# Optimization experiments

Hardware: AMD Instinct MI355X
Metric: run time of the kernel (lower is better)

The kernel has to match this reference:

```python
import jax, jax.numpy as jnp
import numpy as np

MARGIN = 0.5
POS_WEIGHT = 0.5
NEG_WEIGHT = 0.5
PUNISHMENT_SCALE = 2.0
POS_THRESHOLD = 0.6
NEG_THRESHOLD = 0.3
BIG = 1e9  # finite sentinel instead of inf (grad-safe under where)


def setup_inputs() -> dict:
    key = jax.random.key(0)
    k1, k2, k3 = jax.random.split(key, 3)
    N, D = 8192, 256
    embeddings = jax.random.normal(k1, (N, D), dtype=jnp.float32)
    labels = jax.random.randint(k2, (N,), 0, 2, dtype=jnp.int32)
    pids = jax.random.randint(k3, (N,), 0, 256, dtype=jnp.int32)
    return {"embeddings": embeddings, "labels": labels, "pids": pids}


def reference(embeddings, labels, pids):
    N = embeddings.shape[0]
    # F.normalize(p=2, dim=1): x / max(||x||, eps)
    norm = jnp.maximum(jnp.linalg.norm(embeddings, axis=1, keepdims=True), 1e-12)
    normed = embeddings / norm
    sim = normed @ normed.T  # (N, N) cosine similarity

    same_pid = pids[:, None] == pids[None, :]            # (N, N)
    genuine_j = (labels == 1)[None, :]                   # (1, N)
    not_self = ~jnp.eye(N, dtype=bool)
    pos_mask = same_pid & genuine_j & not_self           # same pid, genuine, not anchor
    neg_mask = (same_pid & ~genuine_j) | ~same_pid       # same-pid forgeries or cross-pid

    valid = (labels == 1) & pos_mask.any(axis=1) & neg_mask.any(axis=1)

    # hardest positive = min similarity among positives
    hp = jnp.min(jnp.where(pos_mask, sim, BIG), axis=1)  # (N,)

    # semi-hard negatives: hp - margin < sim < hp
    semi = neg_mask & (sim < hp[:, None]) & (sim > (hp - MARGIN)[:, None])
    cand = neg_mask & (sim > hp[:, None])                # harder-than-positive negatives
    hn_semi = jnp.max(jnp.where(semi, sim, -BIG), axis=1)
    hn_cand = jnp.max(jnp.where(cand, sim, -BIG), axis=1)
    hn_all = jnp.max(jnp.where(neg_mask, sim, -BIG), axis=1)
    hn = jnp.where(semi.any(axis=1), hn_semi,
                   jnp.where(cand.any(axis=1), hn_cand, hn_all))

    base = jax.nn.relu(hn - hp + MARGIN)
    weight = jnp.where((hp < POS_THRESHOLD) | (hn > NEG_THRESHOLD),
                       PUNISHMENT_SCALE, 1.0)
    loss = base * weight + POS_WEIGHT * (1.0 - hp) + NEG_WEIGHT * jax.nn.relu(hn + 0.2)

    cnt = jnp.sum(valid)
    total = jnp.sum(jnp.where(valid, loss, 0.0))
    return jnp.where(cnt > 0, total / jnp.maximum(cnt, 1), 0.0)
```

## Files before the change

### kernel.cpp

```cpp
#include <hip/hip_runtime.h>
#include <hip/hip_bf16.h>
#include <stdint.h>

typedef __attribute__((ext_vector_type(8))) short short8;
typedef __attribute__((ext_vector_type(4))) float f32x4;

#define BIGF 1e9f
#define NSLOT 64
#define MAXM 96

__device__ inline float blo(unsigned int u) {
    union { unsigned int i; float f; } v; v.i = u << 16; return v.f;
}
__device__ inline float bhi(unsigned int u) {
    union { unsigned int i; float f; } v; v.i = u & 0xffff0000u; return v.f;
}
__device__ inline unsigned int fkey(float s) {
    unsigned int b = __float_as_uint(s);
    return (b & 0x80000000u) ? ~b : (b | 0x80000000u);
}
__device__ inline float funkey(unsigned int k) {
    unsigned int b = (k & 0x80000000u) ? (k & 0x7fffffffu) : ~k;
    return __uint_as_float(b);
}
__device__ inline void async16(const unsigned short* g, unsigned short* l) {
    __builtin_amdgcn_global_load_lds(
        (const __attribute__((address_space(1))) void*)g,
        (__attribute__((address_space(3))) void*)l, 16, 0, 0);
}
__device__ inline unsigned short f2b(float x) {
    __hip_bfloat16 h = __float2bfloat16(x);
    return *reinterpret_cast<unsigned short*>(&h);
}

__global__ __launch_bounds__(256) void k_normalize(
    const float* __restrict__ emb, const int* __restrict__ labels,
    const int* __restrict__ pids, unsigned short* __restrict__ normed,
    int* __restrict__ pg, float* __restrict__ hp_init,
    float* __restrict__ gred, int* __restrict__ done)
{
    if (blockIdx.x == 0 && threadIdx.x < 3) {
        if (threadIdx.x < 2) gred[threadIdx.x] = 0.f;
        else *done = 0;
    }
    int w = threadIdx.x >> 6, lane = threadIdx.x & 63;
    int row = blockIdx.x * 4 + w;
    const float4* src = (const float4*)(emb + ((size_t)row << 8));
    float4 x = src[lane];
    float ss = x.x * x.x + x.y * x.y + x.z * x.z + x.w * x.w;
    #pragma unroll
    for (int off = 32; off >= 1; off >>= 1) ss += __shfl_xor(ss, off, 64);
    float inv = 1.0f / fmaxf(sqrtf(ss), 1e-12f);
    ushort4 o;
    o.x = f2b(x.x * inv); o.y = f2b(x.y * inv);
    o.z = f2b(x.z * inv); o.w = f2b(x.w * inv);
    ((ushort4*)(normed + ((size_t)row << 8)))[lane] = o;
    if (lane == 0) {
        int g = (labels[row] == 1) ? pids[row] : -1;
        pg[row] = (pids[row] & 0xffff) | ((g + 1) << 16);
        hp_init[row] = BIGF;
    }
}

__global__ __launch_bounds__(256) void k_hp_pid(
    const unsigned short* __restrict__ normed, const int* __restrict__ labels,
    const int* __restrict__ pids, float* __restrict__ hp_out, int N, int D)
{
    __shared__ int list[MAXM];
    __shared__ unsigned int hp_loc[MAXM];
    __shared__ unsigned short rows[MAXM * 256];
    __shared__ int cnt;
    int p = blockIdx.x;
    int t = threadIdx.x;
    if (t == 0) cnt = 0;
    __syncthreads();
    for (int j = t; j < N; j += 256)
        if (pids[j] == p && labels[j] == 1) {
            int idx = atomicAdd(&cnt, 1);
            if (idx < MAXM) list[idx] = j;
        }
    __syncthreads();
    int M = min(cnt, MAXM);
    for (int s = t; s < M; s += 256) hp_loc[s] = 0xFFFFFFFFu;
    for (int idx = t; idx < M * 32; idx += 256) {
        int mi = idx >> 5, ch = idx & 31;
        ((uint4*)&rows[mi * 256])[ch] =
            ((const uint4*)(normed + ((size_t)list[mi] << 8)))[ch];
    }
    __syncthreads();
    for (int pr = t; pr < M * M; pr += 256) {
        int i = pr / M, j = pr - i * M;
        if (i == j) continue;
        const uint4* ap = (const uint4*)&rows[i * 256];
        const uint4* bp = (const uint4*)&rows[j * 256];
        float s = 0.f;
        #pragma unroll 4
        for (int k = 0; k < 32; ++k) {
            uint4 a = ap[k], b = bp[k];
            s += blo(a.x) * blo(b.x) + bhi(a.x) * bhi(b.x);
            s += blo(a.y) * blo(b.y) + bhi(a.y) * bhi(b.y);
            s += blo(a.z) * blo(b.z) + bhi(a.z) * bhi(b.z);
            s += blo(a.w) * blo(b.w) + bhi(a.w) * bhi(b.w);
        }
        atomicMin(&hp_loc[i], fkey(s));
    }
    __syncthreads();
    for (int s = t; s < M; s += 256) {
        unsigned int key = hp_loc[s];
        hp_out[list[s]] = (key == 0xFFFFFFFFu) ? BIGF : funkey(key);
    }
}

__global__ __launch_bounds__(512) void k_pass2(
    const unsigned short* __restrict__ normed, const int* __restrict__ pg,
    const float* __restrict__ hp,
    float* __restrict__ p_hnall, float* __restrict__ p_mbel, int N)
{
    const int b = blockIdx.x;
    int rt, ct;
    if (b >= 2016) {
        rt = b - 2016; ct = rt;
    } else {
        int r = (int)floorf((127.0f - sqrtf(16129.0f - 8.0f * (float)b)) * 0.5f);
        r = max(0, min(r, 62));
        while (63 * (r + 1) - ((r + 1) * r) / 2 <= b) ++r;
        while (63 * r - (r * (r - 1)) / 2 > b) --r;
        rt = r;
        ct = r + 1 + (b - (63 * r - (r * (r - 1)) / 2));
    }
    const bool diag = (ct == rt);

    __shared__ unsigned short As[2][128 * 32];
    __shared__ unsigned short Bs[2][128 * 32];
    __shared__ float hp_r[128], hp_c[128];
    __shared__ int pg_r[128], pg_c[128];
    __shared__ unsigned int red1[128], red2[128], red3[128], red4[128];

    const int t = threadIdx.x;
    const int lane = t & 63;
    const int w = t >> 6;
    const int wr = w & 3, wc = w >> 2;
    const int quad = lane >> 4, l16 = lane & 15;
    const int rbase = rt * 128, cbase = ct * 128;

    if (t < 128) {
        hp_r[t] = hp[rbase + t];
        pg_r[t] = pg[rbase + t];
        hp_c[t] = hp[cbase + t];
        pg_c[t] = pg[cbase + t];
        red1[t] = 0u; red2[t] = 0u; red3[t] = 0u; red4[t] = 0u;
    }

    const int r0 = t >> 2, p0 = t & 3;
    const int c0 = p0 ^ ((r0 >> 1) & 3);
    const unsigned short* gA = normed + ((size_t)(rbase + r0) << 8) + c0 * 8;
    const unsigned short* gB = normed + ((size_t)(cbase + r0) << 8) + c0 * 8;

    async16(gA, &As[0][t * 8]);
    if (!diag) async16(gB, &Bs[0][t * 8]);

    f32x4 acc[2][4];
    #pragma unroll
    for (int mt = 0; mt < 2; ++mt)
        #pragma unroll
        for (int nt = 0; nt < 4; ++nt)
            acc[mt][nt] = (f32x4){0.f, 0.f, 0.f, 0.f};

    const int sw = (l16 >> 1) & 3;
    const int aoff = (wr * 32 + l16) * 32 + (quad ^ sw) * 8;
    const int boff = (wc * 64 + l16) * 32 + (quad ^ sw) * 8;
    const unsigned short* Bbase[2] = { diag ? &As[0][0] : &Bs[0][0],
                                       diag ? &As[1][0] : &Bs[1][0] };

    for (int kb = 0; kb < 8; ++kb) {
        __syncthreads();
        int cur = kb & 1;
        if (kb < 7) {
            int nxt = cur ^ 1;
            int ko = (kb + 1) << 5;
            async16(gA + ko, &As[nxt][t * 8]);
            if (!diag) async16(gB + ko, &Bs[nxt][t * 8]);
        }
        short8 af[2], bf[4];
        #pragma unroll
        for (int mt = 0; mt < 2; ++mt)
            af[mt] = *reinterpret_cast<const short8*>(&As[cur][aoff + mt * 512]);
        #pragma unroll
        for (int nt = 0; nt < 4; ++nt)
            bf[nt] = *reinterpret_cast<const short8*>(&Bbase[cur][boff + nt * 512]);
        #pragma unroll
        for (int mt = 0; mt < 2; ++mt)
            #pragma unroll
            for (int nt = 0; nt < 4; ++nt)
                acc[mt][nt] = __builtin_amdgcn_mfma_f32_16x16x32_bf16(
                    af[mt], bf[nt], acc[mt][nt], 0, 0, 0);
    }

    {
        const unsigned int gp0 = ((unsigned int)pg_c[wc * 64 +  0 + l16]) >> 16;
        const unsigned int gp1 = ((unsigned int)pg_c[wc * 64 + 16 + l16]) >> 16;
        const unsigned int gp2 = ((unsigned int)pg_c[wc * 64 + 32 + l16]) >> 16;
        const unsigned int gp3 = ((unsigned int)pg_c[wc * 64 + 48 + l16]) >> 16;
        #pragma unroll
        for (int mt = 0; mt < 2; ++mt) {
            #pragma unroll
            for (int r = 0; r < 4; ++r) {
                const int rl = wr * 32 + mt * 16 + quad * 4 + r;
                const unsigned int prP1 = ((unsigned int)pg_r[rl] & 0xffffu) + 1u;
                const float hprow = hp_r[rl];
                float tt0 = (prP1 != gp0) ? acc[mt][0][r] : -BIGF;
                float tt1 = (prP1 != gp1) ? acc[mt][1][r] : -BIGF;
                float tt2 = (prP1 != gp2) ? acc[mt][2][r] : -BIGF;
                float tt3 = (prP1 != gp3) ? acc[mt][3][r] : -BIGF;
                float v1 = fmaxf(fmaxf(tt0, tt1), fmaxf(tt2, tt3));
                float u0 = (tt0 < hprow) ? tt0 : -BIGF;
                float u1 = (tt1 < hprow) ? tt1 : -BIGF;
                float u2 = (tt2 < hprow) ? tt2 : -BIGF;
                float u3 = (tt3 < hprow) ? tt3 : -BIGF;
                float v2 = fmaxf(fmaxf(u0, u1), fmaxf(u2, u3));
                #pragma unroll
                for (int off = 8; off >= 1; off >>= 1) {
                    v1 = fmaxf(v1, __shfl_xor(v1, off, 64));
                    v2 = fmaxf(v2, __shfl_xor(v2, off, 64));
                }
                if (l16 == 0) {
                    atomicMax(&red1[rl], fkey(v1));
                    atomicMax(&red2[rl], fkey(v2));
                }
            }
        }
    }

    if (!diag) {
        #pragma unroll
        for (int nt = 0; nt < 4; ++nt) {
            const int c = wc * 64 + nt * 16 + l16;
            const unsigned int pcP1 = ((unsigned int)pg_c[c] & 0xffffu) + 1u;
            const float hpc = hp_c[c];
            float a1 = -BIGF, b1 = -BIGF;
            #pragma unroll
            for (int mt = 0; mt < 2; ++mt) {
                const int4 pr4 = *(const int4*)&pg_r[wr * 32 + mt * 16 + quad * 4];
                float tt0 = (pcP1 != (((unsigned int)pr4.x) >> 16)) ? acc[mt][nt][0] : -BIGF;
                float tt1 = (pcP1 != (((unsigned int)pr4.y) >> 16)) ? acc[mt][nt][1] : -BIGF;
                float tt2 = (pcP1 != (((unsigned int)pr4.z) >> 16)) ? acc[mt][nt][2] : -BIGF;
                float tt3 = (pcP1 != (((unsigned int)pr4.w) >> 16)) ? acc[mt][nt][3] : -BIGF;
                a1 = fmaxf(a1, fmaxf(fmaxf(tt0, tt1), fmaxf(tt2, tt3)));
                float u0 = (tt0 < hpc) ? tt0 : -BIGF;
                float u1 = (tt1 < hpc) ? tt1 : -BIGF;
                float u2 = (tt2 < hpc) ? tt2 : -BIGF;
                float u3 = (tt3 < hpc) ? tt3 : -BIGF;
                b1 = fmaxf(b1, fmaxf(fmaxf(u0, u1), fmaxf(u2, u3)));
            }
            a1 = fmaxf(a1, __shfl_xor(a1, 16, 64));
            b1 = fmaxf(b1, __shfl_xor(b1, 16, 64));
            a1 = fmaxf(a1, __shfl_xor(a1, 32, 64));
            b1 = fmaxf(b1, __shfl_xor(b1, 32, 64));
            if (quad == 0) {
                atomicMax(&red3[c], fkey(a1));
                atomicMax(&red4[c], fkey(b1));
            }
        }
    }

    __syncthreads();
    if (t < 128) {
        p_hnall[(size_t)ct * N + rbase + t] = funkey(red1[t]);
        p_mbel[(size_t)ct * N + rbase + t] = funkey(red2[t]);
        if (!diag) {
            p_hnall[(size_t)rt * N + cbase + t] = funkey(red3[t]);
            p_mbel[(size_t)rt * N + cbase + t] = funkey(red4[t]);
        }
    }
}

__global__ __launch_bounds__(256) void k_rowloss(
    const float* __restrict__ hp, const float* __restrict__ p_hnall,
    const float* __restrict__ p_mbel, const int* __restrict__ labels,
    float* __restrict__ gred, int* __restrict__ done,
    float* __restrict__ out, int N)
{
    int i = blockIdx.x * 256 + threadIdx.x;
    float hn_all = -BIGF, mb = -BIGF;
    #pragma unroll 8
    for (int s = 0; s < NSLOT; ++s) {
        hn_all = fmaxf(hn_all, p_hnall[(size_t)s * N + i]);
        mb = fmaxf(mb, p_mbel[(size_t)s * N + i]);
    }
    float hpv = hp[i];
    bool valid = (labels[i] == 1) && (hpv < 1e8f) && (hn_all > -1e8f);
    float hn = (mb > hpv - 0.5f) ? mb : hn_all;
    float base = fmaxf(hn - hpv + 0.5f, 0.f);
    float wgt = (hpv < 0.6f || hn > 0.3f) ? 2.f : 1.f;
    float loss = base * wgt + 0.5f * (1.f - hpv) + 0.5f * fmaxf(hn + 0.2f, 0.f);
    float lsum = valid ? loss : 0.f;
    float lcnt = valid ? 1.f : 0.f;
    #pragma unroll
    for (int off = 32; off >= 1; off >>= 1) {
        lsum += __shfl_xor(lsum, off, 64);
        lcnt += __shfl_xor(lcnt, off, 64);
    }
    __shared__ float rs[4], rc[4];
    int wv = threadIdx.x >> 6, lane = threadIdx.x & 63;
    if (lane == 0) { rs[wv] = lsum; rc[wv] = lcnt; }
    __syncthreads();
    if (threadIdx.x == 0) {
        atomicAdd(&gred[0], rs[0] + rs[1] + rs[2] + rs[3]);
        atomicAdd(&gred[1], rc[0] + rc[1] + rc[2] + rc[3]);
        __threadfence();
        int old = atomicAdd(done, 1);
        if (old == (int)gridDim.x - 1) {
            float S = atomicAdd(&gred[0], 0.f);
            float C = atomicAdd(&gred[1], 0.f);
            out[0] = (C > 0.f) ? S / fmaxf(C, 1.f) : 0.f;
        }
    }
}

extern "C" void kernel_launch(void* const* d_in, const int* in_sizes, int n_in,
                              void* d_out, int out_size, void* d_ws, size_t ws_size,
                              hipStream_t stream)
{
    const float* emb = (const float*)d_in[0];
    const int* labels = (const int*)d_in[1];
    const int* pids = (const int*)d_in[2];
    float* out = (float*)d_out;
    int N = in_sizes[1];
    int D = in_sizes[0] / N;

    char* ws = (char*)d_ws;
    unsigned short* normed = (unsigned short*)ws;  ws += (size_t)N * D * 2;
    int* pg = (int*)ws;                            ws += (size_t)N * 4;
    float* hp = (float*)ws;                        ws += (size_t)N * 4;
    float* p_hnall = (float*)ws;                   ws += (size_t)N * NSLOT * 4;
    float* p_mbel = (float*)ws;                    ws += (size_t)N * NSLOT * 4;
    float* gred = (float*)ws;                      ws += 2 * 4;
    int* done = (int*)ws;                          ws += 4;

    int M = N / 128;
    int tri = M * (M + 1) / 2;

    k_normalize<<<N / 4, 256, 0, stream>>>(emb, labels, pids, normed, pg, hp,
                                           gred, done);
    k_hp_pid<<<256, 256, 0, stream>>>(normed, labels, pids, hp, N, D);
    k_pass2<<<tri, 512, 0, stream>>>(normed, pg, hp, p_hnall, p_mbel, N);
    k_rowloss<<<N / 256, 256, 0, stream>>>(hp, p_hnall, p_mbel, labels,
                                           gred, done, out, N);
}
```

Measured before the change: 140.7 us.

## Fuse row-loss reduction into pass2 via global atomics and per-row-tile completion counters

Instead of writing per-slot partial maxima to a 64-slot scratch array and running a separate row-loss kernel, each pass2 block atomically max-merges its row and column results into per-row key arrays. Per-row-tile counters detect the last block touching a tile, and that block computes the loss for the tile's 128 rows and adds it to the global sum. This removes one kernel launch and the 2×N×64 float scratch traffic. In exchange it adds global atomics and a fence in every block, and the result depends on counter and fence correctness.

Measured after the change: 364.8 us. 159% more time.

```diff
diff --git a/kernel.cpp b/kernel.cpp
--- a/kernel.cpp
+++ b/kernel.cpp
@@ -6,7 +6,6 @@
 typedef __attribute__((ext_vector_type(4))) float f32x4;
 
 #define BIGF 1e9f
-#define NSLOT 64
 #define MAXM 96
 
 __device__ inline float blo(unsigned int u) {
@@ -37,11 +36,13 @@
     const float* __restrict__ emb, const int* __restrict__ labels,
     const int* __restrict__ pids, unsigned short* __restrict__ normed,
     int* __restrict__ pg, float* __restrict__ hp_init,
-    float* __restrict__ gred, int* __restrict__ done)
+    unsigned int* __restrict__ hn_key, unsigned int* __restrict__ mb_key,
+    float* __restrict__ gred, int* __restrict__ done, int* __restrict__ done_rt)
 {
-    if (blockIdx.x == 0 && threadIdx.x < 3) {
+    if (blockIdx.x == 0) {
         if (threadIdx.x < 2) gred[threadIdx.x] = 0.f;
-        else *done = 0;
+        else if (threadIdx.x == 2) *done = 0;
+        else if (threadIdx.x >= 4 && threadIdx.x < 68) done_rt[threadIdx.x - 4] = 0;
     }
     int w = threadIdx.x >> 6, lane = threadIdx.x & 63;
     int row = blockIdx.x * 4 + w;
@@ -59,6 +60,8 @@
         int g = (labels[row] == 1) ? pids[row] : -1;
         pg[row] = (pids[row] & 0xffff) | ((g + 1) << 16);
         hp_init[row] = BIGF;
+        hn_key[row] = 0u;
+        mb_key[row] = 0u;
     }
 }
 
@@ -114,7 +117,9 @@
 __global__ __launch_bounds__(512) void k_pass2(
     const unsigned short* __restrict__ normed, const int* __restrict__ pg,
     const float* __restrict__ hp,
-    float* __restrict__ p_hnall, float* __restrict__ p_mbel, int N)
+    unsigned int* __restrict__ hn_key, unsigned int* __restrict__ mb_key,
+    float* __restrict__ gred, int* __restrict__ done, int* __restrict__ done_rt,
+    float* __restrict__ out, int N)
 {
     const int b = blockIdx.x;
     int rt, ct;
@@ -135,6 +140,8 @@
     __shared__ float hp_r[128], hp_c[128];
     __shared__ int pg_r[128], pg_c[128];
     __shared__ unsigned int red1[128], red2[128], red3[128], red4[128];
+    __shared__ float rs2[8], rc2[8];
+    __shared__ int flagsS;
 
     const int t = threadIdx.x;
     const int lane = t & 63;
@@ -265,51 +272,64 @@
 
     __syncthreads();
     if (t < 128) {
-        p_hnall[(size_t)ct * N + rbase + t] = funkey(red1[t]);
-        p_mbel[(size_t)ct * N + rbase + t] = funkey(red2[t]);
+        atomicMax(&hn_key[rbase + t], red1[t]);
+        atomicMax(&mb_key[rbase + t], red2[t]);
         if (!diag) {
-            p_hnall[(size_t)rt * N + cbase + t] = funkey(red3[t]);
-            p_mbel[(size_t)rt * N + cbase + t] = funkey(red4[t]);
-        }
-    }
-}
-
-__global__ __launch_bounds__(256) void k_rowloss(
-    const float* __restrict__ hp, const float* __restrict__ p_hnall,
-    const float* __restrict__ p_mbel, const int* __restrict__ labels,
-    float* __restrict__ gred, int* __restrict__ done,
-    float* __restrict__ out, int N)
-{
-    int i = blockIdx.x * 256 + threadIdx.x;
-    float hn_all = -BIGF, mb = -BIGF;
-    #pragma unroll 8
-    for (int s = 0; s < NSLOT; ++s) {
-        hn_all = fmaxf(hn_all, p_hnall[(size_t)s * N + i]);
-        mb = fmaxf(mb, p_mbel[(size_t)s * N + i]);
-    }
-    float hpv = hp[i];
-    bool valid = (labels[i] == 1) && (hpv < 1e8f) && (hn_all > -1e8f);
-    float hn = (mb > hpv - 0.5f) ? mb : hn_all;
-    float base = fmaxf(hn - hpv + 0.5f, 0.f);
-    float wgt = (hpv < 0.6f || hn > 0.3f) ? 2.f : 1.f;
-    float loss = base * wgt + 0.5f * (1.f - hpv) + 0.5f * fmaxf(hn + 0.2f, 0.f);
-    float lsum = valid ? loss : 0.f;
-    float lcnt = valid ? 1.f : 0.f;
+            atomicMax(&hn_key[cbase + t], red3[t]);
+            atomicMax(&mb_key[cbase + t], red4[t]);
+        }
+    }
+    __threadfence();
+    __syncthreads();
+    if (t == 0) {
+        int f = 0;
+        if (atomicAdd(&done_rt[rt], 1) == 63) f |= 1;
+        if (!diag && atomicAdd(&done_rt[ct], 1) == 63) f |= 2;
+        flagsS = f;
+    }
+    __syncthreads();
+    const int f = flagsS;
+    if (f == 0) return;
+
     #pragma unroll
-    for (int off = 32; off >= 1; off >>= 1) {
-        lsum += __shfl_xor(lsum, off, 64);
-        lcnt += __shfl_xor(lcnt, off, 64);
-    }
-    __shared__ float rs[4], rc[4];
-    int wv = threadIdx.x >> 6, lane = threadIdx.x & 63;
-    if (lane == 0) { rs[wv] = lsum; rc[wv] = lcnt; }
-    __syncthreads();
-    if (threadIdx.x == 0) {
-        atomicAdd(&gred[0], rs[0] + rs[1] + rs[2] + rs[3]);
-        atomicAdd(&gred[1], rc[0] + rc[1] + rc[2] + rc[3]);
+    for (int pass = 0; pass < 2; ++pass) {
+        if (!(f & (pass + 1))) continue;
+        const int g = pass ? ct : rt;
+        float lsum = 0.f, lcnt = 0.f;
+        if (t < 128) {
+            const int row = g * 128 + t;
+            unsigned int hk = atomicMax(&hn_key[row], 0u);
+            unsigned int mk = atomicMax(&mb_key[row], 0u);
+            float hn_all = funkey(hk);
+            float mb = funkey(mk);
+            float hpv = hp[row];
+            bool valid = ((((unsigned int)pg[row]) >> 16) != 0u) &&
+                         (hpv < 1e8f) && (hn_all > -1e8f);
+            float hn = (mb > hpv - 0.5f) ? mb : hn_all;
+            float base = fmaxf(hn - hpv + 0.5f, 0.f);
+            float wgt = (hpv < 0.6f || hn > 0.3f) ? 2.f : 1.f;
+            float loss = base * wgt + 0.5f * (1.f - hpv) + 0.5f * fmaxf(hn + 0.2f, 0.f);
+            lsum = valid ? loss : 0.f;
+            lcnt = valid ? 1.f : 0.f;
+            #pragma unroll
+            for (int off = 32; off >= 1; off >>= 1) {
+                lsum += __shfl_xor(lsum, off, 64);
+                lcnt += __shfl_xor(lcnt, off, 64);
+            }
+            if (lane == 0) { rs2[w] = lsum; rc2[w] = lcnt; }
+        }
+        __syncthreads();
+        if (t == 0) {
+            atomicAdd(&gred[0], rs2[0] + rs2[1]);
+            atomicAdd(&gred[1], rc2[0] + rc2[1]);
+        }
+        __syncthreads();
+    }
+    if (t == 0) {
         __threadfence();
-        int old = atomicAdd(done, 1);
-        if (old == (int)gridDim.x - 1) {
+        const int ng = (f & 1 ? 1 : 0) + (f & 2 ? 1 : 0);
+        int old = atomicAdd(done, ng);
+        if (old + ng == 64) {
             float S = atomicAdd(&gred[0], 0.f);
             float C = atomicAdd(&gred[1], 0.f);
             out[0] = (C > 0.f) ? S / fmaxf(C, 1.f) : 0.f;
@@ -332,18 +352,18 @@
     unsigned short* normed = (unsigned short*)ws;  ws += (size_t)N * D * 2;
     int* pg = (int*)ws;                            ws += (size_t)N * 4;
     float* hp = (float*)ws;                        ws += (size_t)N * 4;
-    float* p_hnall = (float*)ws;                   ws += (size_t)N * NSLOT * 4;
-    float* p_mbel = (float*)ws;                    ws += (size_t)N * NSLOT * 4;
+    unsigned int* hn_key = (unsigned int*)ws;      ws += (size_t)N * 4;
+    unsigned int* mb_key = (unsigned int*)ws;      ws += (size_t)N * 4;
     float* gred = (float*)ws;                      ws += 2 * 4;
     int* done = (int*)ws;                          ws += 4;
+    int* done_rt = (int*)ws;                       ws += 64 * 4;
 
     int M = N / 128;
     int tri = M * (M + 1) / 2;
 
     k_normalize<<<N / 4, 256, 0, stream>>>(emb, labels, pids, normed, pg, hp,
-                                           gred, done);
+                                           hn_key, mb_key, gred, done, done_rt);
     k_hp_pid<<<256, 256, 0, stream>>>(normed, labels, pids, hp, N, D);
-    k_pass2<<<tri, 512, 0, stream>>>(normed, pg, hp, p_hnall, p_mbel, N);
-    k_rowloss<<<N / 256, 256, 0, stream>>>(hp, p_hnall, p_mbel, labels,
-                                           gred, done, out, N);
-}
+    k_pass2<<<tri, 512, 0, stream>>>(normed, pg, hp, hn_key, mb_key,
+                                     gred, done, done_rt, out, N);
+}
```

## Fuse normalize and per-pid hardest-positive kernels into one launch

Applied to the files above, without the earlier changes.

Merges the normalization kernel and the per-pid hardest-positive kernel into a single launch, with the first 2048 blocks normalizing rows and the remaining 256 blocks handling pids. The pid blocks recompute normalization from the raw fp32 embeddings instead of reading the bf16 normed buffer, which removes the dependency between the two stages. This saves one kernel launch and the serialization between them. In exchange it duplicates some normalization work and gives the normalize blocks a large shared-memory footprint, which can reduce their occupancy.

Result: no change. 143.3 us (+1.9%).

```diff
diff --git a/kernel.cpp b/kernel.cpp
--- a/kernel.cpp
+++ b/kernel.cpp
@@ -33,45 +33,46 @@
     return *reinterpret_cast<unsigned short*>(&h);
 }
 
-__global__ __launch_bounds__(256) void k_normalize(
+__global__ __launch_bounds__(256) void k_prep(
     const float* __restrict__ emb, const int* __restrict__ labels,
     const int* __restrict__ pids, unsigned short* __restrict__ normed,
-    int* __restrict__ pg, float* __restrict__ hp_init,
-    float* __restrict__ gred, int* __restrict__ done)
-{
-    if (blockIdx.x == 0 && threadIdx.x < 3) {
-        if (threadIdx.x < 2) gred[threadIdx.x] = 0.f;
-        else *done = 0;
-    }
-    int w = threadIdx.x >> 6, lane = threadIdx.x & 63;
-    int row = blockIdx.x * 4 + w;
-    const float4* src = (const float4*)(emb + ((size_t)row << 8));
-    float4 x = src[lane];
-    float ss = x.x * x.x + x.y * x.y + x.z * x.z + x.w * x.w;
-    #pragma unroll
-    for (int off = 32; off >= 1; off >>= 1) ss += __shfl_xor(ss, off, 64);
-    float inv = 1.0f / fmaxf(sqrtf(ss), 1e-12f);
-    ushort4 o;
-    o.x = f2b(x.x * inv); o.y = f2b(x.y * inv);
-    o.z = f2b(x.z * inv); o.w = f2b(x.w * inv);
-    ((ushort4*)(normed + ((size_t)row << 8)))[lane] = o;
-    if (lane == 0) {
-        int g = (labels[row] == 1) ? pids[row] : -1;
-        pg[row] = (pids[row] & 0xffff) | ((g + 1) << 16);
-        hp_init[row] = BIGF;
-    }
-}
-
-__global__ __launch_bounds__(256) void k_hp_pid(
-    const unsigned short* __restrict__ normed, const int* __restrict__ labels,
-    const int* __restrict__ pids, float* __restrict__ hp_out, int N, int D)
+    int* __restrict__ pg, float* __restrict__ hp,
+    float* __restrict__ gred, int* __restrict__ done, int N)
 {
     __shared__ int list[MAXM];
     __shared__ unsigned int hp_loc[MAXM];
     __shared__ unsigned short rows[MAXM * 256];
     __shared__ int cnt;
-    int p = blockIdx.x;
-    int t = threadIdx.x;
+
+    const int bid = blockIdx.x;
+    const int t = threadIdx.x;
+    const int w = t >> 6, lane = t & 63;
+
+    if (bid < 2048) {
+        if (bid == 0 && t < 3) {
+            if (t < 2) gred[t] = 0.f;
+            else *done = 0;
+        }
+        int row = bid * 4 + w;
+        const float4* src = (const float4*)(emb + ((size_t)row << 8));
+        float4 x = src[lane];
+        float ss = x.x * x.x + x.y * x.y + x.z * x.z + x.w * x.w;
+        #pragma unroll
+        for (int off = 32; off >= 1; off >>= 1) ss += __shfl_xor(ss, off, 64);
+        float inv = 1.0f / fmaxf(sqrtf(ss), 1e-12f);
+        ushort4 o;
+        o.x = f2b(x.x * inv); o.y = f2b(x.y * inv);
+        o.z = f2b(x.z * inv); o.w = f2b(x.w * inv);
+        ((ushort4*)(normed + ((size_t)row << 8)))[lane] = o;
+        if (lane == 0) {
+            int g = (labels[row] == 1) ? pids[row] : -1;
+            pg[row] = (pids[row] & 0xffff) | ((g + 1) << 16);
+            if (labels[row] != 1) hp[row] = BIGF;
+        }
+        return;
+    }
+
+    const int p = bid - 2048;
     if (t == 0) cnt = 0;
     __syncthreads();
     for (int j = t; j < N; j += 256)
@@ -82,10 +83,18 @@
     __syncthreads();
     int M = min(cnt, MAXM);
     for (int s = t; s < M; s += 256) hp_loc[s] = 0xFFFFFFFFu;
-    for (int idx = t; idx < M * 32; idx += 256) {
-        int mi = idx >> 5, ch = idx & 31;
-        ((uint4*)&rows[mi * 256])[ch] =
-            ((const uint4*)(normed + ((size_t)list[mi] << 8)))[ch];
+    for (int s = w; s < M; s += 4) {
+        const int row = list[s];
+        const float4* src = (const float4*)(emb + ((size_t)row << 8));
+        float4 x = src[lane];
+        float ss = x.x * x.x + x.y * x.y + x.z * x.z + x.w * x.w;
+        #pragma unroll
+        for (int off = 32; off >= 1; off >>= 1) ss += __shfl_xor(ss, off, 64);
+        float inv = 1.0f / fmaxf(sqrtf(ss), 1e-12f);
+        ushort4 o;
+        o.x = f2b(x.x * inv); o.y = f2b(x.y * inv);
+        o.z = f2b(x.z * inv); o.w = f2b(x.w * inv);
+        ((ushort4*)&rows[s * 256])[lane] = o;
     }
     __syncthreads();
     for (int pr = t; pr < M * M; pr += 256) {
@@ -107,7 +116,7 @@
     __syncthreads();
     for (int s = t; s < M; s += 256) {
         unsigned int key = hp_loc[s];
-        hp_out[list[s]] = (key == 0xFFFFFFFFu) ? BIGF : funkey(key);
+        hp[list[s]] = (key == 0xFFFFFFFFu) ? BIGF : funkey(key);
     }
 }
 
@@ -327,9 +336,10 @@
     float* out = (float*)d_out;
     int N = in_sizes[1];
     int D = in_sizes[0] / N;
+    (void)D;
 
     char* ws = (char*)d_ws;
-    unsigned short* normed = (unsigned short*)ws;  ws += (size_t)N * D * 2;
+    unsigned short* normed = (unsigned short*)ws;  ws += (size_t)N * 256 * 2;
     int* pg = (int*)ws;                            ws += (size_t)N * 4;
     float* hp = (float*)ws;                        ws += (size_t)N * 4;
     float* p_hnall = (float*)ws;                   ws += (size_t)N * NSLOT * 4;
@@ -340,9 +350,8 @@
     int M = N / 128;
     int tri = M * (M + 1) / 2;
 
-    k_normalize<<<N / 4, 256, 0, stream>>>(emb, labels, pids, normed, pg, hp,
-                                           gred, done);
-    k_hp_pid<<<256, 256, 0, stream>>>(normed, labels, pids, hp, N, D);
+    k_prep<<<2048 + 256, 256, 0, stream>>>(emb, labels, pids, normed, pg, hp,
+                                           gred, done, N);
     k_pass2<<<tri, 512, 0, stream>>>(normed, pg, hp, p_hnall, p_mbel, N);
     k_rowloss<<<N / 256, 256, 0, stream>>>(hp, p_hnall, p_mbel, labels,
                                            gred, done, out, N);
```

## Replace LDS atomicMax row/col reductions with shared partial buffers; widen rowloss grid

Applied to the files above, without the earlier changes.

The pass-2 epilogue no longer does shuffle trees and LDS atomicMax on key-encoded floats. Each lane writes its partial max pair into a padded float2 buffer that reuses the tile smem, then 4 threads per row finish with a short loop and two shuffles. The rowloss kernel now splits the 64 slots across 8 thread groups per row with 32 rows per block, giving 8x more blocks to parallelise the strided slot reads. This adds extra __syncthreads and more global atomics on the done counter.

Measured after the change: 131.7 us. 1.07x faster.

```diff
diff --git a/kernel.cpp b/kernel.cpp
--- a/kernel.cpp
+++ b/kernel.cpp
@@ -130,11 +130,11 @@
     }
     const bool diag = (ct == rt);
 
-    __shared__ unsigned short As[2][128 * 32];
-    __shared__ unsigned short Bs[2][128 * 32];
+    __shared__ __align__(16) unsigned char smem[33792];
+    unsigned short (*As)[4096] = (unsigned short (*)[4096])(smem);
+    unsigned short (*Bs)[4096] = (unsigned short (*)[4096])(smem + 16384);
     __shared__ float hp_r[128], hp_c[128];
     __shared__ int pg_r[128], pg_c[128];
-    __shared__ unsigned int red1[128], red2[128], red3[128], red4[128];
 
     const int t = threadIdx.x;
     const int lane = t & 63;
@@ -148,7 +148,6 @@
         pg_r[t] = pg[rbase + t];
         hp_c[t] = hp[cbase + t];
         pg_c[t] = pg[cbase + t];
-        red1[t] = 0u; red2[t] = 0u; red3[t] = 0u; red4[t] = 0u;
     }
 
     const int r0 = t >> 2, p0 = t & 3;
@@ -196,7 +195,11 @@
                     af[mt], bf[nt], acc[mt][nt], 0, 0, 0);
     }
 
+    __syncthreads();
+
+    float2 (*part)[33] = (float2 (*)[33])smem;
     {
+        const int cs = wc * 16 + l16;
         const unsigned int gp0 = ((unsigned int)pg_c[wc * 64 +  0 + l16]) >> 16;
         const unsigned int gp1 = ((unsigned int)pg_c[wc * 64 + 16 + l16]) >> 16;
         const unsigned int gp2 = ((unsigned int)pg_c[wc * 64 + 32 + l16]) >> 16;
@@ -218,20 +221,33 @@
                 float u2 = (tt2 < hprow) ? tt2 : -BIGF;
                 float u3 = (tt3 < hprow) ? tt3 : -BIGF;
                 float v2 = fmaxf(fmaxf(u0, u1), fmaxf(u2, u3));
-                #pragma unroll
-                for (int off = 8; off >= 1; off >>= 1) {
-                    v1 = fmaxf(v1, __shfl_xor(v1, off, 64));
-                    v2 = fmaxf(v2, __shfl_xor(v2, off, 64));
-                }
-                if (l16 == 0) {
-                    atomicMax(&red1[rl], fkey(v1));
-                    atomicMax(&red2[rl], fkey(v2));
-                }
-            }
+                part[rl][cs] = float2{v1, v2};
+            }
+        }
+    }
+    __syncthreads();
+
+    {
+        const int row = t >> 2, seg = t & 3;
+        float v1 = -BIGF, v2 = -BIGF;
+        #pragma unroll
+        for (int k = 0; k < 8; ++k) {
+            float2 p = part[row][seg * 8 + k];
+            v1 = fmaxf(v1, p.x); v2 = fmaxf(v2, p.y);
+        }
+        v1 = fmaxf(v1, __shfl_xor(v1, 1, 64));
+        v2 = fmaxf(v2, __shfl_xor(v2, 1, 64));
+        v1 = fmaxf(v1, __shfl_xor(v1, 2, 64));
+        v2 = fmaxf(v2, __shfl_xor(v2, 2, 64));
+        if (seg == 0) {
+            p_hnall[(size_t)ct * N + rbase + row] = v1;
+            p_mbel [(size_t)ct * N + rbase + row] = v2;
         }
     }
 
     if (!diag) {
+        __syncthreads();
+        float2 (*tpart)[17] = (float2 (*)[17])smem;
         #pragma unroll
         for (int nt = 0; nt < 4; ++nt) {
             const int c = wc * 64 + nt * 16 + l16;
@@ -252,24 +268,25 @@
                 float u3 = (tt3 < hpc) ? tt3 : -BIGF;
                 b1 = fmaxf(b1, fmaxf(fmaxf(u0, u1), fmaxf(u2, u3)));
             }
-            a1 = fmaxf(a1, __shfl_xor(a1, 16, 64));
-            b1 = fmaxf(b1, __shfl_xor(b1, 16, 64));
-            a1 = fmaxf(a1, __shfl_xor(a1, 32, 64));
-            b1 = fmaxf(b1, __shfl_xor(b1, 32, 64));
-            if (quad == 0) {
-                atomicMax(&red3[c], fkey(a1));
-                atomicMax(&red4[c], fkey(b1));
-            }
-        }
-    }
-
-    __syncthreads();
-    if (t < 128) {
-        p_hnall[(size_t)ct * N + rbase + t] = funkey(red1[t]);
-        p_mbel[(size_t)ct * N + rbase + t] = funkey(red2[t]);
-        if (!diag) {
-            p_hnall[(size_t)rt * N + cbase + t] = funkey(red3[t]);
-            p_mbel[(size_t)rt * N + cbase + t] = funkey(red4[t]);
+            tpart[c][wr * 4 + quad] = float2{a1, b1};
+        }
+        __syncthreads();
+        {
+            const int c = t >> 2, sg = t & 3;
+            float a = -BIGF, bm = -BIGF;
+            #pragma unroll
+            for (int k = 0; k < 4; ++k) {
+                float2 p = tpart[c][sg * 4 + k];
+                a = fmaxf(a, p.x); bm = fmaxf(bm, p.y);
+            }
+            a  = fmaxf(a,  __shfl_xor(a,  1, 64));
+            bm = fmaxf(bm, __shfl_xor(bm, 1, 64));
+            a  = fmaxf(a,  __shfl_xor(a,  2, 64));
+            bm = fmaxf(bm, __shfl_xor(bm, 2, 64));
+            if (sg == 0) {
+                p_hnall[(size_t)rt * N + cbase + c] = a;
+                p_mbel [(size_t)rt * N + cbase + c] = bm;
+            }
         }
     }
 }
@@ -280,39 +297,48 @@
     float* __restrict__ gred, int* __restrict__ done,
     float* __restrict__ out, int N)
 {
-    int i = blockIdx.x * 256 + threadIdx.x;
+    const int t = threadIdx.x;
+    const int r = blockIdx.x * 32 + (t & 31);
+    const int g = t >> 5;
     float hn_all = -BIGF, mb = -BIGF;
-    #pragma unroll 8
-    for (int s = 0; s < NSLOT; ++s) {
-        hn_all = fmaxf(hn_all, p_hnall[(size_t)s * N + i]);
-        mb = fmaxf(mb, p_mbel[(size_t)s * N + i]);
-    }
-    float hpv = hp[i];
-    bool valid = (labels[i] == 1) && (hpv < 1e8f) && (hn_all > -1e8f);
-    float hn = (mb > hpv - 0.5f) ? mb : hn_all;
-    float base = fmaxf(hn - hpv + 0.5f, 0.f);
-    float wgt = (hpv < 0.6f || hn > 0.3f) ? 2.f : 1.f;
-    float loss = base * wgt + 0.5f * (1.f - hpv) + 0.5f * fmaxf(hn + 0.2f, 0.f);
-    float lsum = valid ? loss : 0.f;
-    float lcnt = valid ? 1.f : 0.f;
     #pragma unroll
-    for (int off = 32; off >= 1; off >>= 1) {
-        lsum += __shfl_xor(lsum, off, 64);
-        lcnt += __shfl_xor(lcnt, off, 64);
-    }
-    __shared__ float rs[4], rc[4];
-    int wv = threadIdx.x >> 6, lane = threadIdx.x & 63;
-    if (lane == 0) { rs[wv] = lsum; rc[wv] = lcnt; }
-    __syncthreads();
-    if (threadIdx.x == 0) {
-        atomicAdd(&gred[0], rs[0] + rs[1] + rs[2] + rs[3]);
-        atomicAdd(&gred[1], rc[0] + rc[1] + rc[2] + rc[3]);
-        __threadfence();
-        int old = atomicAdd(done, 1);
-        if (old == (int)gridDim.x - 1) {
-            float S = atomicAdd(&gred[0], 0.f);
-            float C = atomicAdd(&gred[1], 0.f);
-            out[0] = (C > 0.f) ? S / fmaxf(C, 1.f) : 0.f;
+    for (int k = 0; k < 8; ++k) {
+        const int s = g * 8 + k;
+        hn_all = fmaxf(hn_all, p_hnall[(size_t)s * N + r]);
+        mb     = fmaxf(mb,     p_mbel [(size_t)s * N + r]);
+    }
+    hn_all = fmaxf(hn_all, __shfl_xor(hn_all, 32, 64));
+    mb     = fmaxf(mb,     __shfl_xor(mb,     32, 64));
+    __shared__ float shn[4][32], smb[4][32];
+    const int w = t >> 6, l = t & 63;
+    if (l < 32) { shn[w][l] = hn_all; smb[w][l] = mb; }
+    __syncthreads();
+    if (t < 32) {
+        float hn1 = fmaxf(fmaxf(shn[0][t], shn[1][t]), fmaxf(shn[2][t], shn[3][t]));
+        float mb1 = fmaxf(fmaxf(smb[0][t], smb[1][t]), fmaxf(smb[2][t], smb[3][t]));
+        float hpv = hp[r];
+        bool valid = (labels[r] == 1) && (hpv < 1e8f) && (hn1 > -1e8f);
+        float hn = (mb1 > hpv - 0.5f) ? mb1 : hn1;
+        float base = fmaxf(hn - hpv + 0.5f, 0.f);
+        float wgt = (hpv < 0.6f || hn > 0.3f) ? 2.f : 1.f;
+        float loss = base * wgt + 0.5f * (1.f - hpv) + 0.5f * fmaxf(hn + 0.2f, 0.f);
+        float lsum = valid ? loss : 0.f;
+        float lcnt = valid ? 1.f : 0.f;
+        #pragma unroll
+        for (int off = 16; off >= 1; off >>= 1) {
+            lsum += __shfl_xor(lsum, off, 64);
+            lcnt += __shfl_xor(lcnt, off, 64);
+        }
+        if (t == 0) {
+            atomicAdd(&gred[0], lsum);
+            atomicAdd(&gred[1], lcnt);
+            __threadfence();
+            int old = atomicAdd(done, 1);
+            if (old == (int)gridDim.x - 1) {
+                float S = atomicAdd(&gred[0], 0.f);
+                float C = atomicAdd(&gred[1], 0.f);
+                out[0] = (C > 0.f) ? S / fmaxf(C, 1.f) : 0.f;
+            }
         }
     }
 }
@@ -344,6 +370,6 @@
                                            gred, done);
     k_hp_pid<<<256, 256, 0, stream>>>(normed, labels, pids, hp, N, D);
     k_pass2<<<tri, 512, 0, stream>>>(normed, pg, hp, p_hnall, p_mbel, N);
-    k_rowloss<<<N / 256, 256, 0, stream>>>(hp, p_hnall, p_mbel, labels,
-                                           gred, done, out, N);
-}
+    k_rowloss<<<N / 32, 256, 0, stream>>>(hp, p_hnall, p_mbel, labels,
+                                          gred, done, out, N);
+}
```
